# Kernel tuning notes

Hardware: AMD Instinct MI355X
Metric: run time of the kernel (lower is better)

## Reference

```python
import jax, jax.numpy as jnp
import numpy as np

N_NODES = 50000
N_EDGES = 800000


def _gat_conv(x, src, dst, W, att_src, att_dst, bias, heads, out_ch, concat, num_nodes):
    # x: [N, d_in]; W: [d_in, heads*out_ch]; att_*: [heads, out_ch]; bias: [heads*out_ch] or [out_ch]
    xh = (x @ W).reshape(num_nodes, heads, out_ch)          # [N, H, C]
    a_src = jnp.einsum('nhc,hc->nh', xh, att_src)            # [N, H]
    a_dst = jnp.einsum('nhc,hc->nh', xh, att_dst)            # [N, H]
    e = jax.nn.leaky_relu(a_src[src] + a_dst[dst], 0.2)      # [E, H]
    # segment softmax over incoming edges per destination node
    m = jax.ops.segment_max(e, dst, num_segments=num_nodes)  # [N, H]
    ex = jnp.exp(e - m[dst])                                  # [E, H]
    denom = jax.ops.segment_sum(ex, dst, num_segments=num_nodes)  # [N, H]
    coeff = ex / denom[dst]                                   # [E, H]
    # scatter-add aggregation of attention-weighted source features
    out = jax.ops.segment_sum(coeff[:, :, None] * xh[src], dst, num_segments=num_nodes)  # [N, H, C]
    if concat:
        out = out.reshape(num_nodes, heads * out_ch)
    else:
        out = out.mean(axis=1)
    return out + bias


def setup_inputs() -> dict:
    key = jax.random.key(0)
    ks = jax.random.split(key, 10)
    d_in, h1, heads, d_out = 64, 64, 4, 128
    X = jax.random.normal(ks[0], (N_NODES, d_in), dtype=jnp.float32)
    edge_index = jax.random.randint(ks[1], (2, N_EDGES), 0, N_NODES, dtype=jnp.int32)
    s1 = 1.0 / np.sqrt(d_in)
    s2 = 1.0 / np.sqrt(heads * h1)
    return {
        'X': X,
        'edge_index': edge_index,
        'W1': jax.random.normal(ks[2], (d_in, heads * h1), dtype=jnp.float32) * s1,
        'att_src1': jax.random.normal(ks[3], (heads, h1), dtype=jnp.float32) * s2,
        'att_dst1': jax.random.normal(ks[4], (heads, h1), dtype=jnp.float32) * s2,
        'b1': jnp.zeros((heads * h1,), dtype=jnp.float32),
        'W2': jax.random.normal(ks[5], (heads * h1, d_out), dtype=jnp.float32) * s2,
        'att_src2': jax.random.normal(ks[6], (1, d_out), dtype=jnp.float32) * 0.1,
        'att_dst2': jax.random.normal(ks[7], (1, d_out), dtype=jnp.float32) * 0.1,
        'b2': jnp.zeros((d_out,), dtype=jnp.float32),
    }


def reference(X, edge_index, W1, att_src1, att_dst1, b1, W2, att_src2, att_dst2, b2):
    num_nodes = X.shape[0]
    loops = jnp.arange(num_nodes, dtype=edge_index.dtype)
    src = jnp.concatenate([edge_index[0], loops])  # add_self_loops=True
    dst = jnp.concatenate([edge_index[1], loops])
    H = _gat_conv(X, src, dst, W1, att_src1, att_dst1, b1, heads=4, out_ch=64, concat=True, num_nodes=num_nodes)
    H = _gat_conv(H, src, dst, W2, att_src2, att_dst2, b2, heads=1, out_ch=128, concat=False, num_nodes=num_nodes)
    return H
```

## Files before the change

kernel.cpp:

```cpp
#include <hip/hip_runtime.h>
#include <hip/hip_bf16.h>
#include <hip/hip_fp16.h>

typedef float v4 __attribute__((ext_vector_type(4)));
typedef _Float16 hv8 __attribute__((ext_vector_type(8)));
typedef _Float16 h2 __attribute__((ext_vector_type(2)));
typedef unsigned int u32x4 __attribute__((ext_vector_type(4)));
typedef unsigned short u16x4 __attribute__((ext_vector_type(4)));

#define BCAP 8192
#define NCAP 64

__device__ __forceinline__ unsigned short f2h(float f) {
    _Float16 h = (_Float16)f;
    return __builtin_bit_cast(unsigned short, h);
}
__device__ __forceinline__ void unph8(uint4 u, v4& lo, v4& hi) {
    h2 a = __builtin_bit_cast(h2, u.x);
    h2 b = __builtin_bit_cast(h2, u.y);
    h2 c = __builtin_bit_cast(h2, u.z);
    h2 d = __builtin_bit_cast(h2, u.w);
    lo[0] = (float)a[0]; lo[1] = (float)a[1]; lo[2] = (float)b[0]; lo[3] = (float)b[1];
    hi[0] = (float)c[0]; hi[1] = (float)c[1]; hi[2] = (float)d[0]; hi[3] = (float)d[1];
}
__device__ __forceinline__ float leaky02(float x) { return x >= 0.f ? x : 0.2f * x; }


__global__ __launch_bounds__(256) void prep_kernel(
    const float* __restrict__ X, const float* __restrict__ W1, const float* __restrict__ W2,
    const float* __restrict__ as1, const float* __restrict__ ad1,
    const int* __restrict__ src, const int* __restrict__ dst,
    int* __restrict__ bucketCnt, unsigned* __restrict__ binned,
    unsigned short* __restrict__ Xh, unsigned short* __restrict__ W1T,
    unsigned short* __restrict__ W2T,
    float* __restrict__ a_src1, float* __restrict__ a_dst1,
    int XB, int NX, int E, int T, int BINB, int N)
{
    int b = blockIdx.x, t = threadIdx.x;
    if (b < XB) {
        int i = (b * 256 + t) * 8;
        if (i < NX) {
            float4 a = *(const float4*)&X[i];
            float4 c = *(const float4*)&X[i + 4];
            ushort4 r0; r0.x = f2h(a.x); r0.y = f2h(a.y); r0.z = f2h(a.z); r0.w = f2h(a.w);
            ushort4 r1; r1.x = f2h(c.x); r1.y = f2h(c.y); r1.z = f2h(c.z); r1.w = f2h(c.w);
            *(ushort4*)&Xh[i] = r0;
            *(ushort4*)&Xh[i + 4] = r1;
        }
    } else if (b < XB + 64) {
        int id = (b - XB) * 256 + t;
        int j = id >> 6, k = id & 63;
        W1T[id] = f2h(W1[k * 256 + j]);
    } else if (b < XB + 192) {
        int id = (b - XB - 64) * 256 + t;
        int j = id >> 8, k = id & 255;
        W2T[id] = f2h(W2[k * 128 + j]);
    } else if (b < XB + 192 + BINB) {
        __shared__ int cnt[256];
        __shared__ int basep[256];
        cnt[t] = 0; __syncthreads();
        int base = (b - XB - 192) * 2048;
        unsigned pv[8]; int bk[8], rv[8];
        #pragma unroll
        for (int j = 0; j < 8; j++) {
            int id = base + j * 256 + t;
            if (id < T) {
                int ss, dd;
                if (id < E) { ss = src[id]; dd = dst[id]; }
                else        { ss = dd = id - E; }
                bk[j] = dd >> 8;
                pv[j] = ((unsigned)(dd & 255) << 24) | (unsigned)ss;
                rv[j] = atomicAdd(&cnt[bk[j]], 1);
            } else bk[j] = -1;
        }
        __syncthreads();
        int v = cnt[t];
        if (v) basep[t] = t * BCAP + atomicAdd(&bucketCnt[t], v);
        __syncthreads();
        #pragma unroll
        for (int j = 0; j < 8; j++) {
            if (bk[j] >= 0)
                binned[basep[bk[j]] + rv[j]] = pv[j];
        }
    } else {
        __shared__ float vs[256], vd[256];
        {
            int h = t >> 6, k = t & 63;
            const float* wrow = &W1[k * 256 + h * 64];
            const float* ar = &as1[h * 64];
            const float* dr = &ad1[h * 64];
            float sv = 0.f, dv = 0.f;
            #pragma unroll 8
            for (int c = 0; c < 64; c++) { sv += wrow[c] * ar[c]; dv += wrow[c] * dr[c]; }
            vs[t] = sv; vd[t] = dv;
        }
        __syncthreads();
        int w = t >> 6, lane = t & 63;
        int nd = lane >> 3, sub = lane & 7, kc = sub * 8;
        int node = (b - XB - 192 - BINB) * 32 + w * 8 + nd;
        if (node >= N) node = N - 1;
        float4 xlo = *(const float4*)&X[(size_t)node * 64 + kc];
        float4 xhi = *(const float4*)&X[(size_t)node * 64 + kc + 4];
        float ps[4], pd[4];
        #pragma unroll
        for (int h = 0; h < 4; h++) {
            const float* vsh = &vs[h * 64 + kc];
            const float* vdh = &vd[h * 64 + kc];
            float s = xlo.x * vsh[0] + xlo.y * vsh[1] + xlo.z * vsh[2] + xlo.w * vsh[3]
                    + xhi.x * vsh[4] + xhi.y * vsh[5] + xhi.z * vsh[6] + xhi.w * vsh[7];
            float d = xlo.x * vdh[0] + xlo.y * vdh[1] + xlo.z * vdh[2] + xlo.w * vdh[3]
                    + xhi.x * vdh[4] + xhi.y * vdh[5] + xhi.z * vdh[6] + xhi.w * vdh[7];
            ps[h] = s; pd[h] = d;
        }
        #pragma unroll
        for (int off = 1; off < 8; off <<= 1)
            #pragma unroll
            for (int h = 0; h < 4; h++) {
                ps[h] += __shfl_xor(ps[h], off);
                pd[h] += __shfl_xor(pd[h], off);
            }
        if (sub == 0) {
            v4 o0; o0[0] = ps[0]; o0[1] = ps[1]; o0[2] = ps[2]; o0[3] = ps[3];
            v4 o1; o1[0] = pd[0]; o1[1] = pd[1]; o1[2] = pd[2]; o1[3] = pd[3];
            *(v4*)&a_src1[node * 4] = o0;
            *(v4*)&a_dst1[node * 4] = o1;
        }
    }
}


__global__ __launch_bounds__(256) void place_kernel(
    const int* __restrict__ bucketCnt, const unsigned* __restrict__ binned,
    int* __restrict__ counts, int* __restrict__ csr_src, int N)
{
    __shared__ int cur[256];
    int b = blockIdx.x, t = threadIdx.x;
    cur[t] = 0; __syncthreads();
    int beg = b * BCAP, end = beg + bucketCnt[b];
    int nb0 = b * 256;
    for (int i = beg + t; i < end; i += 256) {
        unsigned u = binned[i];
        int dl = u >> 24;
        int s  = (int)(u & 0xFFFFFF);
        int r = atomicAdd(&cur[dl], 1);
        if (r < NCAP) csr_src[(size_t)(nb0 + dl) * NCAP + r] = s;
    }
    __syncthreads();
    int n = nb0 + t;
    if (n < N) {
        int c = cur[t]; if (c > NCAP) c = NCAP;
        counts[n] = c;
        int cp = (c + 7) & ~7;
        size_t o = (size_t)n * NCAP;
        for (int q = c; q < cp; q++) csr_src[o + q] = n;
    }
}


__global__ __launch_bounds__(256) void aggGemm_kernel(
    const int* __restrict__ counts, const int* __restrict__ csr_src,
    const float* __restrict__ a_src1, const float* __restrict__ a_dst1,
    const unsigned short* __restrict__ Xh, const unsigned short* __restrict__ W1T,
    const float* __restrict__ b1, const unsigned short* __restrict__ W2T,
    const float* __restrict__ att_src, const float* __restrict__ att_dst,
    unsigned short* __restrict__ xh2, float* __restrict__ a_src2, float* __restrict__ a_dst2,
    int N)
{
    __shared__ unsigned short As[64 * 264];
    __shared__ unsigned short Ws[256 * 72];
    int t  = threadIdx.x;
    int n0 = blockIdx.x * 64;
    int wid = t >> 6, lane = t & 63;
    int quad = lane >> 4, lm = lane & 15;

    {
        int nd = lane >> 5;
        int hl = lane & 31;
        int p = (lane >> 3) & 3, sub = lane & 7, kc = sub * 8;
        float* fb = (float*)Ws;
        float (*wn)[4] = (float(*)[4])(fb + (wid * 2 + nd) * 256);
        int*   sn      = (int*)(fb + 2048) + (wid * 2 + nd) * 64;

        for (int it = 0; it < 8; it++) {
            int lrow = wid * 16 + it * 2 + nd;
            int n = n0 + lrow;
            int nc = n < N ? n : N - 1;
            int cnt  = counts[nc];
            int degp = (cnt + 7) & ~7;
            size_t beg = (size_t)nc * NCAP;
            int L = degp;
            v4 adst = *(const v4*)&a_dst1[nc * 4];

            v4 den = (v4)0.f;
            for (int q = hl; q < L; q += 32) {
                int s = __builtin_nontemporal_load(&csr_src[beg + q]);
                v4 a = *(const v4*)&a_src1[s * 4];
                v4 wv;
                #pragma unroll
                for (int h = 0; h < 4; h++) {
                    float e = fminf(leaky02(a[h] + adst[h]), 80.f);
                    wv[h] = (q < cnt) ? __expf(e) : 0.f;
                }
                *(v4*)wn[q] = wv;
                sn[q] = s;
                den += wv;
            }
            #pragma unroll
            for (int off = 1; off < 32; off <<= 1)
                #pragma unroll
                for (int h = 0; h < 4; h++) den[h] += __shfl_xor(den[h], off);

            v4 accL[4], accH[4];
            #pragma unroll
            for (int h = 0; h < 4; h++) { accL[h] = (v4)0.f; accH[h] = (v4)0.f; }

            int steps = L >> 2;
            auto sidx = [&](int i) { int j = i < steps ? i : steps - 1; return j * 4 + p; };
            int sa_ = sn[sidx(0)], sb_ = sn[sidx(1)];
            uint4 xa = *(const uint4*)&Xh[(size_t)sa_ * 64 + kc];
            uint4 xb = *(const uint4*)&Xh[(size_t)sb_ * 64 + kc];
            for (int i = 0; i < steps; i++) {
                int sc_ = sn[sidx(i + 2)];
                uint4 xc = *(const uint4*)&Xh[(size_t)sc_ * 64 + kc];
                v4 w = *(const v4*)wn[i * 4 + p];
                v4 lo, hi; unph8(xa, lo, hi);
                #pragma unroll
                for (int h = 0; h < 4; h++) { accL[h] += w[h] * lo; accH[h] += w[h] * hi; }
                xa = xb; xb = xc;
            }

            #pragma unroll
            for (int off = 8; off < 32; off <<= 1) {
                #pragma unroll
                for (int h = 0; h < 4; h++) {
                    #pragma unroll
                    for (int c = 0; c < 4; c++) {
                        accL[h][c] += __shfl_xor(accL[h][c], off);
                        accH[h][c] += __shfl_xor(accH[h][c], off);
                    }
                }
            }
            if (p == 0) {
                #pragma unroll
                for (int h = 0; h < 4; h++) {
                    float inv = 1.f / den[h];
                    v4 oL = accL[h] * inv, oH = accH[h] * inv;
                    u32x4 pk;
                    pk[0] = (unsigned)f2h(oL[0]) | ((unsigned)f2h(oL[1]) << 16);
                    pk[1] = (unsigned)f2h(oL[2]) | ((unsigned)f2h(oL[3]) << 16);
                    pk[2] = (unsigned)f2h(oH[0]) | ((unsigned)f2h(oH[1]) << 16);
                    pk[3] = (unsigned)f2h(oH[2]) | ((unsigned)f2h(oH[3]) << 16);
                    *(u32x4*)&As[lrow * 264 + h * 64 + kc] = pk;
                }
            }
        }
    }
    __syncthreads();

    #pragma unroll
    for (int c = 0; c < 8; c++) {
        int idx = c * 256 + t;
        int row = idx >> 3, seg = idx & 7;
        *(uint4*)&Ws[row * 72 + seg * 8] = *(const uint4*)&W1T[row * 64 + seg * 8];
    }
    __syncthreads();

    v4 hacc[2][8];
    #pragma unroll
    for (int r = 0; r < 2; r++) {
        int tl = wid * 2 + r;
        int nq = tl & 3, th = tl >> 2;
        hv8 xf0[2], xf1[2];
        #pragma unroll
        for (int hh = 0; hh < 2; hh++) {
            int h = th * 2 + hh;
            xf0[hh] = *(const hv8*)&As[(nq * 16 + lm) * 264 + h * 64 + quad * 8];
            xf1[hh] = *(const hv8*)&As[(nq * 16 + lm) * 264 + h * 64 + 32 + quad * 8];
        }
        #pragma unroll
        for (int tt2 = 0; tt2 < 8; tt2++) {
            int tt = th * 8 + tt2;
            int hh = tt2 >> 2;
            hv8 wf0 = *(const hv8*)&Ws[(tt * 16 + lm) * 72 + quad * 8];
            hv8 wf1 = *(const hv8*)&Ws[(tt * 16 + lm) * 72 + 32 + quad * 8];
            v4 a = (v4)0.f;
            a = __builtin_amdgcn_mfma_f32_16x16x32_f16(wf0, xf0[hh], a, 0, 0, 0);
            a = __builtin_amdgcn_mfma_f32_16x16x32_f16(wf1, xf1[hh], a, 0, 0, 0);
            int ch = tt * 16 + quad * 4;
            v4 bias = *(const v4*)&b1[ch];
            hacc[r][tt2] = a + bias;
        }
    }
    __syncthreads();
    #pragma unroll
    for (int r = 0; r < 2; r++) {
        int tl = wid * 2 + r;
        int nq = tl & 3, th = tl >> 2;
        #pragma unroll
        for (int tt2 = 0; tt2 < 8; tt2++) {
            int tt = th * 8 + tt2;
            int ch = tt * 16 + quad * 4;
            v4 o = hacc[r][tt2];
            u16x4 b;
            b[0] = f2h(o[0]); b[1] = f2h(o[1]); b[2] = f2h(o[2]); b[3] = f2h(o[3]);
            *(u16x4*)&As[(nq * 16 + lm) * 264 + ch] = b;
        }
    }

    v4 acc[8];
    #pragma unroll
    for (int tt = 0; tt < 8; tt++) acc[tt] = (v4)0.f;
    for (int kt = 0; kt < 256; kt += 64) {
        __syncthreads();
        #pragma unroll
        for (int c = 0; c < 4; c++) {
            int idx = c * 256 + t;
            int row = idx >> 3, seg = idx & 7;
            *(uint4*)&Ws[row * 72 + seg * 8] = *(const uint4*)&W2T[row * 256 + kt + seg * 8];
        }
        __syncthreads();

        hv8 xf0 = *(const hv8*)&As[(wid * 16 + lm) * 264 + kt + quad * 8];
        hv8 xf1 = *(const hv8*)&As[(wid * 16 + lm) * 264 + kt + 32 + quad * 8];
        #pragma unroll
        for (int tt = 0; tt < 8; tt++) {
            hv8 wf0 = *(const hv8*)&Ws[(tt * 16 + lm) * 72 + quad * 8];
            hv8 wf1 = *(const hv8*)&Ws[(tt * 16 + lm) * 72 + 32 + quad * 8];
            acc[tt] = __builtin_amdgcn_mfma_f32_16x16x32_f16(wf0, xf0, acc[tt], 0, 0, 0);
            acc[tt] = __builtin_amdgcn_mfma_f32_16x16x32_f16(wf1, xf1, acc[tt], 0, 0, 0);
        }
    }

    int node = n0 + wid * 16 + lm;
    float vs = 0.f, vd = 0.f;
    #pragma unroll
    for (int tt = 0; tt < 8; tt++) {
        int ch = tt * 16 + quad * 4;
        v4 d = acc[tt];
        v4 as_ = *(const v4*)&att_src[ch];
        v4 ad_ = *(const v4*)&att_dst[ch];
        #pragma unroll
        for (int r = 0; r < 4; r++) { vs += d[r] * as_[r]; vd += d[r] * ad_[r]; }
        ushort4 b; b.x = f2h(d[0]); b.y = f2h(d[1]); b.z = f2h(d[2]); b.w = f2h(d[3]);
        if (node < N) *(ushort4*)&xh2[(size_t)node * 128 + ch] = b;
    }
    vs += __shfl_xor(vs, 16); vs += __shfl_xor(vs, 32);
    vd += __shfl_xor(vd, 16); vd += __shfl_xor(vd, 32);
    if (lane < 16 && node < N) { a_src2[node] = vs; a_dst2[node] = vd; }
}


__global__ __launch_bounds__(256) void aggf2_kernel(
    const int* __restrict__ counts, const int* __restrict__ csr_src,
    const float* __restrict__ a_src2, const float* __restrict__ a_dst2,
    const unsigned short* __restrict__ xh2, const float* __restrict__ b2,
    float* __restrict__ out, int N)
{
    __shared__ float wlds[4][2][64];
    __shared__ int   slds[4][2][64];
    int wid  = threadIdx.x >> 6;
    int lane = threadIdx.x & 63;
    int nd = lane >> 5;
    int hl = lane & 31;
    int p = (lane >> 4) & 1;
    int c0 = (lane & 15) * 8;
    int n = blockIdx.x * 8 + wid * 2 + nd;
    if (n >= N) return;
    int cnt  = counts[n];
    int degp = (cnt + 7) & ~7;
    size_t beg = (size_t)n * NCAP;
    int L = degp;
    float adst = a_dst2[n];
    float* wn = wlds[wid][nd];
    int*   sn = slds[wid][nd];

    float den = 0.f;
    for (int q = hl; q < L; q += 32) {
        int s = __builtin_nontemporal_load(&csr_src[beg + q]);
        float a = a_src2[s];
        float e = fminf(leaky02(a + adst), 80.f);
        float w = (q < cnt) ? __expf(e) : 0.f;
        wn[q] = w; sn[q] = s;
        den += w;
    }
    #pragma unroll
    for (int off = 1; off < 32; off <<= 1) den += __shfl_xor(den, off);

    v4 accL = (v4)0.f, accH = (v4)0.f;
    int steps = L >> 1;
    auto sidx = [&](int i) { int j = i < steps ? i : steps - 1; return j * 2 + p; };
    int sa_ = sn[sidx(0)], sb_ = sn[sidx(1)];
    uint4 xa = *(const uint4*)&xh2[(size_t)sa_ * 128 + c0];
    uint4 xb = *(const uint4*)&xh2[(size_t)sb_ * 128 + c0];
    for (int i = 0; i < steps; i++) {
        int sc_ = sn[sidx(i + 2)];
        uint4 xc = *(const uint4*)&xh2[(size_t)sc_ * 128 + c0];
        float w = wn[i * 2 + p];
        v4 lo, hi; unph8(xa, lo, hi);
        accL += w * lo; accH += w * hi;
        xa = xb; xb = xc;
    }

    #pragma unroll
    for (int c = 0; c < 4; c++) {
        accL[c] += __shfl_xor(accL[c], 16);
        accH[c] += __shfl_xor(accH[c], 16);
    }
    if (p == 0) {
        float inv = 1.f / den;
        v4 bl = *(const v4*)&b2[c0];
        v4 bh = *(const v4*)&b2[c0 + 4];
        v4 oL = accL * inv + bl;
        v4 oH = accH * inv + bh;
        __builtin_nontemporal_store(oL, (v4*)&out[(size_t)n * 128 + c0]);
        __builtin_nontemporal_store(oH, (v4*)&out[(size_t)n * 128 + c0 + 4]);
    }
}


static inline size_t rnd256(size_t x) { return (x + 255) & ~(size_t)255; }

extern "C" void kernel_launch(void* const* d_in, const int* in_sizes, int n_in,
                              void* d_out, int out_size, void* d_ws, size_t ws_size,
                              hipStream_t stream) {
    const float* X   = (const float*)d_in[0];
    const int*   ei  = (const int*)d_in[1];
    const float* W1  = (const float*)d_in[2];
    const float* as1 = (const float*)d_in[3];
    const float* ad1 = (const float*)d_in[4];
    const float* b1  = (const float*)d_in[5];
    const float* W2  = (const float*)d_in[6];
    const float* as2 = (const float*)d_in[7];
    const float* ad2 = (const float*)d_in[8];
    const float* b2  = (const float*)d_in[9];
    float* out = (float*)d_out;

    const int N = in_sizes[0] / 64;
    const int E = in_sizes[1] / 2;
    const int T = E + N;
    const int NBUK = (N + 255) >> 8;
    const int* srcArr = ei;
    const int* dstArr = ei + E;
    const int XB = (N * 64 / 8 + 255) / 256;
    const int BINB = (T + 2047) / 2048;
    const int ATTB = (N + 31) / 32;

    char* w = (char*)d_ws;
    unsigned short* Xh     = (unsigned short*)w;  w += rnd256((size_t)N * 64 * 2);
    unsigned short* W1T    = (unsigned short*)w;  w += rnd256((size_t)256 * 64 * 2);
    unsigned short* W2T    = (unsigned short*)w;  w += rnd256((size_t)128 * 256 * 2);
    unsigned short* xh2    = (unsigned short*)w;  w += rnd256((size_t)N * 128 * 2);
    float* a_src1  = (float*)w;  w += rnd256((size_t)N * 4 * 4);
    float* a_dst1  = (float*)w;  w += rnd256((size_t)N * 4 * 4);
    float* a_src2v = (float*)w;  w += rnd256((size_t)N * 4);
    float* a_dst2v = (float*)w;  w += rnd256((size_t)N * 4);
    int*   counts  = (int*)w;    w += rnd256((size_t)N * 4);
    int*   bucketCnt = (int*)w;  w += rnd256(256 * 4);
    unsigned* binned = (unsigned*)w; w += rnd256((size_t)NBUK * BCAP * 4);
    int*   csr_src = (int*)w;    w += rnd256((size_t)NBUK * 256 * NCAP * 4);

    hipMemsetAsync(bucketCnt, 0, 256 * sizeof(int), stream);
    prep_kernel<<<XB + 192 + BINB + ATTB, 256, 0, stream>>>(
        X, W1, W2, as1, ad1, srcArr, dstArr, bucketCnt, binned,
        Xh, W1T, W2T, a_src1, a_dst1, XB, N * 64, E, T, BINB, N);
    place_kernel<<<NBUK, 256, 0, stream>>>(bucketCnt, binned, counts, csr_src, N);
    aggGemm_kernel<<<(N + 63) / 64, 256, 0, stream>>>(counts, csr_src, a_src1, a_dst1,
                                                      Xh, W1T, b1, W2T, as2, ad2,
                                                      xh2, a_src2v, a_dst2v, N);
    aggf2_kernel<<<(N + 7) / 8, 256, 0, stream>>>(counts, csr_src, a_src2v, a_dst2v,
                                                  xh2, b2, out, N);
}
```

Baseline: 230.9 us.

## Split fused layer-1 aggregation+GEMM kernel into separate gather and GEMM kernels

Moves the attention-weighted neighbor aggregation out of the fused kernel into its own kernel with 8 nodes per block. It writes the aggregated fp16 features to a new global buffer, which a separate GEMM kernel then loads into LDS. The goal is more parallelism and occupancy for the latency-bound gather, which previously ran serially over 64 nodes per block ahead of the MFMA work. The cost is an extra kernel launch and a global write and read of roughly 25 MB of intermediate data.

```diff
diff --git a/kernel.cpp b/kernel.cpp
--- a/kernel.cpp
+++ b/kernel.cpp
@@ -157,10 +157,95 @@
 }
 
 
-__global__ __launch_bounds__(256) void aggGemm_kernel(
+__global__ __launch_bounds__(256) void aggX_kernel(
     const int* __restrict__ counts, const int* __restrict__ csr_src,
     const float* __restrict__ a_src1, const float* __restrict__ a_dst1,
-    const unsigned short* __restrict__ Xh, const unsigned short* __restrict__ W1T,
+    const unsigned short* __restrict__ Xh, unsigned short* __restrict__ Xagg, int N)
+{
+    __shared__ float wlds[4][2][64][4];
+    __shared__ int   slds[4][2][64];
+    int wid  = threadIdx.x >> 6;
+    int lane = threadIdx.x & 63;
+    int nd = lane >> 5;
+    int hl = lane & 31;
+    int p = (lane >> 3) & 3, sub = lane & 7, kc = sub * 8;
+    int n = blockIdx.x * 8 + wid * 2 + nd;
+    if (n >= N) return;
+    int cnt  = counts[n];
+    int degp = (cnt + 7) & ~7;
+    size_t beg = (size_t)n * NCAP;
+    int L = degp;
+    v4 adst = *(const v4*)&a_dst1[n * 4];
+    float (*wn)[4] = wlds[wid][nd];
+    int* sn = slds[wid][nd];
+
+    v4 den = (v4)0.f;
+    for (int q = hl; q < L; q += 32) {
+        int s = __builtin_nontemporal_load(&csr_src[beg + q]);
+        v4 a = *(const v4*)&a_src1[s * 4];
+        v4 wv;
+        #pragma unroll
+        for (int h = 0; h < 4; h++) {
+            float e = fminf(leaky02(a[h] + adst[h]), 80.f);
+            wv[h] = (q < cnt) ? __expf(e) : 0.f;
+        }
+        *(v4*)wn[q] = wv;
+        sn[q] = s;
+        den += wv;
+    }
+    #pragma unroll
+    for (int off = 1; off < 32; off <<= 1)
+        #pragma unroll
+        for (int h = 0; h < 4; h++) den[h] += __shfl_xor(den[h], off);
+
+    v4 accL[4], accH[4];
+    #pragma unroll
+    for (int h = 0; h < 4; h++) { accL[h] = (v4)0.f; accH[h] = (v4)0.f; }
+
+    int steps = L >> 2;
+    auto sidx = [&](int i) { int j = i < steps ? i : steps - 1; return j * 4 + p; };
+    int sa_ = sn[sidx(0)], sb_ = sn[sidx(1)];
+    uint4 xa = *(const uint4*)&Xh[(size_t)sa_ * 64 + kc];
+    uint4 xb = *(const uint4*)&Xh[(size_t)sb_ * 64 + kc];
+    for (int i = 0; i < steps; i++) {
+        int sc_ = sn[sidx(i + 2)];
+        uint4 xc = *(const uint4*)&Xh[(size_t)sc_ * 64 + kc];
+        v4 w = *(const v4*)wn[i * 4 + p];
+        v4 lo, hi; unph8(xa, lo, hi);
+        #pragma unroll
+        for (int h = 0; h < 4; h++) { accL[h] += w[h] * lo; accH[h] += w[h] * hi; }
+        xa = xb; xb = xc;
+    }
+
+    #pragma unroll
+    for (int off = 8; off < 32; off <<= 1) {
+        #pragma unroll
+        for (int h = 0; h < 4; h++) {
+            #pragma unroll
+            for (int c = 0; c < 4; c++) {
+                accL[h][c] += __shfl_xor(accL[h][c], off);
+                accH[h][c] += __shfl_xor(accH[h][c], off);
+            }
+        }
+    }
+    if (p == 0) {
+        #pragma unroll
+        for (int h = 0; h < 4; h++) {
+            float inv = 1.f / den[h];
+            v4 oL = accL[h] * inv, oH = accH[h] * inv;
+            u32x4 pk;
+            pk[0] = (unsigned)f2h(oL[0]) | ((unsigned)f2h(oL[1]) << 16);
+            pk[1] = (unsigned)f2h(oL[2]) | ((unsigned)f2h(oL[3]) << 16);
+            pk[2] = (unsigned)f2h(oH[0]) | ((unsigned)f2h(oH[1]) << 16);
+            pk[3] = (unsigned)f2h(oH[2]) | ((unsigned)f2h(oH[3]) << 16);
+            __builtin_nontemporal_store(pk, (u32x4*)&Xagg[(size_t)n * 256 + h * 64 + kc]);
+        }
+    }
+}
+
+
+__global__ __launch_bounds__(256) void gemmHW2_kernel(
+    const unsigned short* __restrict__ Xagg, const unsigned short* __restrict__ W1T,
     const float* __restrict__ b1, const unsigned short* __restrict__ W2T,
     const float* __restrict__ att_src, const float* __restrict__ att_dst,
     unsigned short* __restrict__ xh2, float* __restrict__ a_src2, float* __restrict__ a_dst2,
@@ -170,93 +255,16 @@
     __shared__ unsigned short Ws[256 * 72];
     int t  = threadIdx.x;
     int n0 = blockIdx.x * 64;
-    int wid = t >> 6, lane = t & 63;
-    int quad = lane >> 4, lm = lane & 15;
-
-    {
-        int nd = lane >> 5;
-        int hl = lane & 31;
-        int p = (lane >> 3) & 3, sub = lane & 7, kc = sub * 8;
-        float* fb = (float*)Ws;
-        float (*wn)[4] = (float(*)[4])(fb + (wid * 2 + nd) * 256);
-        int*   sn      = (int*)(fb + 2048) + (wid * 2 + nd) * 64;
-
-        for (int it = 0; it < 8; it++) {
-            int lrow = wid * 16 + it * 2 + nd;
-            int n = n0 + lrow;
-            int nc = n < N ? n : N - 1;
-            int cnt  = counts[nc];
-            int degp = (cnt + 7) & ~7;
-            size_t beg = (size_t)nc * NCAP;
-            int L = degp;
-            v4 adst = *(const v4*)&a_dst1[nc * 4];
-
-            v4 den = (v4)0.f;
-            for (int q = hl; q < L; q += 32) {
-                int s = __builtin_nontemporal_load(&csr_src[beg + q]);
-                v4 a = *(const v4*)&a_src1[s * 4];
-                v4 wv;
-                #pragma unroll
-                for (int h = 0; h < 4; h++) {
-                    float e = fminf(leaky02(a[h] + adst[h]), 80.f);
-                    wv[h] = (q < cnt) ? __expf(e) : 0.f;
-                }
-                *(v4*)wn[q] = wv;
-                sn[q] = s;
-                den += wv;
-            }
-            #pragma unroll
-            for (int off = 1; off < 32; off <<= 1)
-                #pragma unroll
-                for (int h = 0; h < 4; h++) den[h] += __shfl_xor(den[h], off);
-
-            v4 accL[4], accH[4];
-            #pragma unroll
-            for (int h = 0; h < 4; h++) { accL[h] = (v4)0.f; accH[h] = (v4)0.f; }
-
-            int steps = L >> 2;
-            auto sidx = [&](int i) { int j = i < steps ? i : steps - 1; return j * 4 + p; };
-            int sa_ = sn[sidx(0)], sb_ = sn[sidx(1)];
-            uint4 xa = *(const uint4*)&Xh[(size_t)sa_ * 64 + kc];
-            uint4 xb = *(const uint4*)&Xh[(size_t)sb_ * 64 + kc];
-            for (int i = 0; i < steps; i++) {
-                int sc_ = sn[sidx(i + 2)];
-                uint4 xc = *(const uint4*)&Xh[(size_t)sc_ * 64 + kc];
-                v4 w = *(const v4*)wn[i * 4 + p];
-                v4 lo, hi; unph8(xa, lo, hi);
-                #pragma unroll
-                for (int h = 0; h < 4; h++) { accL[h] += w[h] * lo; accH[h] += w[h] * hi; }
-                xa = xb; xb = xc;
-            }
-
-            #pragma unroll
-            for (int off = 8; off < 32; off <<= 1) {
-                #pragma unroll
-                for (int h = 0; h < 4; h++) {
-                    #pragma unroll
-                    for (int c = 0; c < 4; c++) {
-                        accL[h][c] += __shfl_xor(accL[h][c], off);
-                        accH[h][c] += __shfl_xor(accH[h][c], off);
-                    }
-                }
-            }
-            if (p == 0) {
-                #pragma unroll
-                for (int h = 0; h < 4; h++) {
-                    float inv = 1.f / den[h];
-                    v4 oL = accL[h] * inv, oH = accH[h] * inv;
-                    u32x4 pk;
-                    pk[0] = (unsigned)f2h(oL[0]) | ((unsigned)f2h(oL[1]) << 16);
-                    pk[1] = (unsigned)f2h(oL[2]) | ((unsigned)f2h(oL[3]) << 16);
-                    pk[2] = (unsigned)f2h(oH[0]) | ((unsigned)f2h(oH[1]) << 16);
-                    pk[3] = (unsigned)f2h(oH[2]) | ((unsigned)f2h(oH[3]) << 16);
-                    *(u32x4*)&As[lrow * 264 + h * 64 + kc] = pk;
-                }
-            }
-        }
-    }
-    __syncthreads();
-
+    int w = t >> 6, l = t & 63;
+    int quad = l >> 4, lm = l & 15;
+
+    #pragma unroll
+    for (int c = 0; c < 8; c++) {
+        int idx = c * 256 + t;
+        int row = idx >> 5, seg = idx & 31;
+        int gr = n0 + row; if (gr >= N) gr = N - 1;
+        *(uint4*)&As[row * 264 + seg * 8] = *(const uint4*)&Xagg[(size_t)gr * 256 + seg * 8];
+    }
     #pragma unroll
     for (int c = 0; c < 8; c++) {
         int idx = c * 256 + t;
@@ -268,7 +276,7 @@
     v4 hacc[2][8];
     #pragma unroll
     for (int r = 0; r < 2; r++) {
-        int tl = wid * 2 + r;
+        int tl = w * 2 + r;
         int nq = tl & 3, th = tl >> 2;
         hv8 xf0[2], xf1[2];
         #pragma unroll
@@ -294,7 +302,7 @@
     __syncthreads();
     #pragma unroll
     for (int r = 0; r < 2; r++) {
-        int tl = wid * 2 + r;
+        int tl = w * 2 + r;
         int nq = tl & 3, th = tl >> 2;
         #pragma unroll
         for (int tt2 = 0; tt2 < 8; tt2++) {
@@ -320,8 +328,8 @@
         }
         __syncthreads();
 
-        hv8 xf0 = *(const hv8*)&As[(wid * 16 + lm) * 264 + kt + quad * 8];
-        hv8 xf1 = *(const hv8*)&As[(wid * 16 + lm) * 264 + kt + 32 + quad * 8];
+        hv8 xf0 = *(const hv8*)&As[(w * 16 + lm) * 264 + kt + quad * 8];
+        hv8 xf1 = *(const hv8*)&As[(w * 16 + lm) * 264 + kt + 32 + quad * 8];
         #pragma unroll
         for (int tt = 0; tt < 8; tt++) {
             hv8 wf0 = *(const hv8*)&Ws[(tt * 16 + lm) * 72 + quad * 8];
@@ -331,7 +339,7 @@
         }
     }
 
-    int node = n0 + wid * 16 + lm;
+    int node = n0 + w * 16 + lm;
     float vs = 0.f, vd = 0.f;
     #pragma unroll
     for (int tt = 0; tt < 8; tt++) {
@@ -346,7 +354,7 @@
     }
     vs += __shfl_xor(vs, 16); vs += __shfl_xor(vs, 32);
     vd += __shfl_xor(vd, 16); vd += __shfl_xor(vd, 32);
-    if (lane < 16 && node < N) { a_src2[node] = vs; a_dst2[node] = vd; }
+    if (l < 16 && node < N) { a_src2[node] = vs; a_dst2[node] = vd; }
 }
 
 
@@ -449,6 +457,7 @@
     unsigned short* Xh     = (unsigned short*)w;  w += rnd256((size_t)N * 64 * 2);
     unsigned short* W1T    = (unsigned short*)w;  w += rnd256((size_t)256 * 64 * 2);
     unsigned short* W2T    = (unsigned short*)w;  w += rnd256((size_t)128 * 256 * 2);
+    unsigned short* Xagg   = (unsigned short*)w;  w += rnd256((size_t)N * 256 * 2);
     unsigned short* xh2    = (unsigned short*)w;  w += rnd256((size_t)N * 128 * 2);
     float* a_src1  = (float*)w;  w += rnd256((size_t)N * 4 * 4);
     float* a_dst1  = (float*)w;  w += rnd256((size_t)N * 4 * 4);
@@ -464,8 +473,9 @@
         X, W1, W2, as1, ad1, srcArr, dstArr, bucketCnt, binned,
         Xh, W1T, W2T, a_src1, a_dst1, XB, N * 64, E, T, BINB, N);
     place_kernel<<<NBUK, 256, 0, stream>>>(bucketCnt, binned, counts, csr_src, N);
-    aggGemm_kernel<<<(N + 63) / 64, 256, 0, stream>>>(counts, csr_src, a_src1, a_dst1,
-                                                      Xh, W1T, b1, W2T, as2, ad2,
+    aggX_kernel<<<(N + 7) / 8, 256, 0, stream>>>(counts, csr_src, a_src1, a_dst1,
+                                                 Xh, Xagg, N);
+    gemmHW2_kernel<<<(N + 63) / 64, 256, 0, stream>>>(Xagg, W1T, b1, W2T, as2, ad2,
                                                       xh2, a_src2v, a_dst2v, N);
     aggf2_kernel<<<(N + 7) / 8, 256, 0, stream>>>(counts, csr_src, a_src2v, a_dst2v,
                                                   xh2, b2, out, N);
```

Result: faster. 210.5 us (-8.8%).
